# Kernel optimization log

Hardware: AMD Instinct MI355X
Metric: run time of the kernel (lower is better)

Reference implementation:

```python
import jax, jax.numpy as jnp
import numpy as np

N = 50000        # nodes
E = 800000       # edges (before self loops)
F_IN = 78        # num_features_xd
H1 = 10          # heads of gcn1
OUT2 = 128       # output_dim of gcn2
G = 512          # graphs in batch
NEG_SLOPE = 0.2  # PyG GATConv default


def setup_inputs() -> dict:
    key = jax.random.key(0)
    ks = jax.random.split(key, 16)
    def glorot(k, shape, fan_in):
        return jax.random.normal(k, shape, jnp.float32) * (1.0 / np.sqrt(fan_in))
    inp = {}
    inp['x'] = jax.random.normal(ks[0], (N, F_IN), jnp.float32)
    inp['edge_index'] = jax.random.randint(ks[1], (2, E), 0, N, dtype=jnp.int32)
    inp['batch'] = jnp.sort(jax.random.randint(ks[2], (N,), 0, G, dtype=jnp.int32))
    inp['num_graphs'] = G
    # gcn1: GATConv(78 -> 78, heads=10, concat=True)
    inp['W1'] = glorot(ks[3], (F_IN, H1 * F_IN), F_IN)
    inp['a_src1'] = glorot(ks[4], (H1, F_IN), F_IN)
    inp['a_dst1'] = glorot(ks[5], (H1, F_IN), F_IN)
    inp['b1'] = jnp.zeros((H1 * F_IN,), jnp.float32)
    # gcn2: GATConv(780 -> 128, heads=1)
    inp['W2'] = glorot(ks[6], (H1 * F_IN, OUT2), H1 * F_IN)
    inp['a_src2'] = glorot(ks[7], (1, OUT2), OUT2)
    inp['a_dst2'] = glorot(ks[8], (1, OUT2), OUT2)
    inp['b2'] = jnp.zeros((OUT2,), jnp.float32)
    # fc_g1: Linear(128 -> 128)
    inp['fcW'] = glorot(ks[9], (OUT2, OUT2), OUT2)
    inp['fcb'] = jnp.zeros((OUT2,), jnp.float32)
    return inp


def _gat_layer(x, src, dst, W, a_src, a_dst, b, heads, out_dim):
    # x: [N, Fin] -> h: [N, heads, out_dim]
    n = x.shape[0]
    h = (x @ W).reshape(n, heads, out_dim)
    # per-node attention projections: [N, heads]
    alpha_src = jnp.einsum('nhf,hf->nh', h, a_src)
    alpha_dst = jnp.einsum('nhf,hf->nh', h, a_dst)
    # per-edge logits (message from src j to dst i): [Etot, heads]
    e = jax.nn.leaky_relu(alpha_src[src] + alpha_dst[dst], NEG_SLOPE)
    # segment softmax over edges grouped by destination node
    m = jax.ops.segment_max(e, dst, num_segments=n)
    m = jnp.where(jnp.isfinite(m), m, 0.0)
    ex = jnp.exp(e - m[dst])
    denom = jax.ops.segment_sum(ex, dst, num_segments=n)
    alpha = ex / (denom[dst] + 1e-16)
    # weighted message scatter: [N, heads, out_dim]
    out = jax.ops.segment_sum(h[src] * alpha[:, :, None], dst, num_segments=n)
    return out.reshape(n, heads * out_dim) + b


def reference(x, edge_index, batch, num_graphs, W1, a_src1, a_dst1, b1,
              W2, a_src2, a_dst2, b2, fcW, fcb):
    n = x.shape[0]
    # PyG GATConv add_self_loops=True
    loops = jnp.arange(n, dtype=edge_index.dtype)
    src = jnp.concatenate([edge_index[0], loops])
    dst = jnp.concatenate([edge_index[1], loops])
    # eval mode: dropouts are identity
    h = jax.nn.relu(_gat_layer(x, src, dst, W1, a_src1, a_dst1, b1, H1, F_IN))
    h = jax.nn.relu(_gat_layer(h, src, dst, W2, a_src2, a_dst2, b2, 1, OUT2))
    # global max pool over graphs
    pooled = jax.ops.segment_max(h, batch, num_segments=num_graphs)
    pooled = jnp.where(jnp.isfinite(pooled), pooled, 0.0)
    return jax.nn.relu(pooled @ fcW + fcb)
```

## Files before the change

kernel.cpp:

```cpp
#include <hip/hip_runtime.h>
#include <hip/hip_bf16.h>
#include <stdint.h>

typedef unsigned int uint32;
typedef unsigned short u16;
typedef __attribute__((ext_vector_type(8))) short bf16x8;
typedef __attribute__((ext_vector_type(4))) float f32x4;
typedef __attribute__((ext_vector_type(2))) float f32x2;
typedef uint32 u32x4 __attribute__((ext_vector_type(4)));

#define N_NODES 50000
#define NP      50048
#define N_EDGES 800000
#define ETOT    (N_EDGES + N_NODES)
#define F_INN   78
#define H1      10
#define D1      780
#define OUT2    128
#define NGRAPH  512
#define NEG_SLOPE 0.2f
#define PL40    ((size_t)NP * 40)

__device__ __forceinline__ float lrelu(float v) { return v > 0.f ? v : NEG_SLOPE * v; }
__device__ __forceinline__ u16 f2bfbits(float f) {
    return __bfloat16_as_ushort(__float2bfloat16(f));
}
__device__ __forceinline__ uint32 packbf(float lo, float hi) {
    return (uint32)f2bfbits(lo) | ((uint32)f2bfbits(hi) << 16);
}
__device__ __forceinline__ f32x2 bf2(uint32 u) {
    __hip_bfloat162 b = *reinterpret_cast<__hip_bfloat162*>(&u);
    float2 t = __bfloat1622float2(b);
    return (f32x2){t.x, t.y};
}
__device__ __forceinline__ int esrc(const int* ei, int e) { return e < N_EDGES ? ei[e] : e - N_EDGES; }
__device__ __forceinline__ int edst(const int* ei, int e) { return e < N_EDGES ? ei[N_EDGES + e] : e - N_EDGES; }

typedef __attribute__((address_space(1))) const uint32 guint;
typedef __attribute__((address_space(3))) uint32 luint;
__device__ __forceinline__ void cp16(uint32* lds, const uint32* g, int lane) {
    __builtin_amdgcn_global_load_lds((guint*)(g + lane * 4), (luint*)lds, 16, 0, 0);
}

#define NXP (N_NODES * 80)
__global__ __launch_bounds__(256) void prep_kernel(const float* __restrict__ x,
                                                   const float* __restrict__ W1,
                                                   const float* __restrict__ W2,
                                                   u16* __restrict__ xbp,
                                                   u16* __restrict__ w1p,
                                                   u16* __restrict__ w2p) {
    const int total = NXP + 10 * 80 * 80 + 10 * 128 * 80;
    for (int id = blockIdx.x * 256 + threadIdx.x; id < total; id += gridDim.x * 256) {
        if (id < NXP) {
            int n = id / 80, k = id - n * 80;
            xbp[id] = (k < 78) ? f2bfbits(x[n * 78 + k]) : ((k == 78) ? (u16)0x3F80 : (u16)0);
        } else if (id < NXP + 64000) {
            int t = id - NXP;
            int h = t / 6400, r = t - h * 6400;
            int n = r / 80, k = r - n * 80;
            w1p[t] = (n < 78 && k < 78) ? f2bfbits(W1[k * D1 + h * 78 + n]) : (u16)0;
        } else {
            int t = id - NXP - 64000;
            int h = t / 10240, r = t - h * 10240;
            int n = r / 80, k = r - n * 80;
            w2p[t] = (k < 78) ? f2bfbits(W2[(h * 78 + k) * OUT2 + n]) : (u16)0;
        }
    }
}

__global__ __launch_bounds__(256) void prep2_kernel(const float* __restrict__ W1,
                                                    const float* __restrict__ a_src1,
                                                    const float* __restrict__ a_dst1,
                                                    const float* __restrict__ W2,
                                                    const float* __restrict__ a_src2,
                                                    const float* __restrict__ a_dst2,
                                                    u16* __restrict__ VAT,
                                                    float* __restrict__ w2as,
                                                    float* __restrict__ w2ad) {
    int gid = blockIdx.x * 256 + threadIdx.x;
    int gs = gridDim.x * 256;
    for (int idx = gid; idx < 32 * 80; idx += gs) {
        int j = idx / 80, k = idx - j * 80;
        float s = 0.f;
        if (j < 20 && k < 78) {
            int h = (j < 10) ? j : j - 10;
            const float* vec = ((j < 10) ? a_src1 : a_dst1) + h * F_INN;
            const float* wrow = W1 + k * D1 + h * F_INN;
            for (int f = 0; f < F_INN; ++f) s = fmaf(wrow[f], vec[f], s);
            VAT[idx] = f2bfbits(s);
        } else {
            VAT[idx] = 0;
        }
    }
    for (int c = gid; c < D1; c += gs) {
        const float* r0 = W2 + (size_t)c * OUT2;
        float s = 0.f, d = 0.f;
        for (int j = 0; j < OUT2; ++j) {
            s = fmaf(r0[j], a_src2[j], s);
            d = fmaf(r0[j], a_dst2[j], d);
        }
        w2as[c] = s;
        w2ad[c] = d;
    }
}

__global__ __launch_bounds__(256) void alphas1x_kernel(const uint32* __restrict__ xbu,
                                                       const uint32* __restrict__ vatu,
                                                       float* __restrict__ asd1,
                                                       float* __restrict__ asrc) {
    __shared__ uint32 As[5136];
    __shared__ uint32 Bs[1296];
    int tid = threadIdx.x, lane = tid & 63, wv = tid >> 6;
    int row0 = blockIdx.x * 128;
    const uint32* aplane = xbu + (size_t)row0 * 40;

#pragma unroll
    for (int t = 0; t < 5; ++t)
        cp16(As + wv * 1280 + t * 256, aplane + wv * 1280 + t * 256, lane);
    if (wv == 0) {
#pragma unroll
        for (int t = 0; t < 5; ++t)
            cp16(Bs + t * 256, vatu + t * 256, lane);
    }
    __syncthreads();

    int l15 = lane & 15, quad = lane >> 4;
    const u16* Asu = (const u16*)As;
    const u16* Bsu = (const u16*)Bs;
    f32x4 acc[2][2];
#pragma unroll
    for (int mi = 0; mi < 2; ++mi)
#pragma unroll
        for (int nj = 0; nj < 2; ++nj) acc[mi][nj] = (f32x4){0.f, 0.f, 0.f, 0.f};

    int abase[2], bbase[2];
#pragma unroll
    for (int mi = 0; mi < 2; ++mi) abase[mi] = (wv * 32 + mi * 16 + l15) * 80 + quad * 8;
#pragma unroll
    for (int nj = 0; nj < 2; ++nj) bbase[nj] = (nj * 16 + l15) * 80 + quad * 8;

    bf16x8 z8 = {0, 0, 0, 0, 0, 0, 0, 0};
#pragma unroll
    for (int ks = 0; ks < 96; ks += 32) {
        bf16x8 a[2], b[2];
#pragma unroll
        for (int mi = 0; mi < 2; ++mi) {
            a[mi] = *(const bf16x8*)(Asu + abase[mi] + ks);
            if (ks == 64 && quad >= 2) a[mi] = z8;
        }
#pragma unroll
        for (int nj = 0; nj < 2; ++nj) b[nj] = *(const bf16x8*)(Bsu + bbase[nj] + ks);
#pragma unroll
        for (int mi = 0; mi < 2; ++mi)
#pragma unroll
            for (int nj = 0; nj < 2; ++nj)
                acc[mi][nj] = __builtin_amdgcn_mfma_f32_16x16x32_bf16(a[mi], b[nj], acc[mi][nj], 0, 0, 0);
    }

#pragma unroll
    for (int mi = 0; mi < 2; ++mi)
#pragma unroll
        for (int nj = 0; nj < 2; ++nj) {
            int col = nj * 16 + l15;
            if (col < 20) {
#pragma unroll
                for (int reg = 0; reg < 4; ++reg) {
                    int row = row0 + wv * 32 + mi * 16 + quad * 4 + reg;
                    if (row < N_NODES) {
                        asd1[(size_t)row * 20 + col] = acc[mi][nj][reg];
                        if (col < 10) asrc[(size_t)row * 12 + col] = acc[mi][nj][reg];
                    }
                }
            }
        }
}

__global__ void histrank_kernel(const int* __restrict__ ei, int* __restrict__ deg,
                                int* __restrict__ rank) {
    int e = blockIdx.x * 256 + threadIdx.x;
    if (e < ETOT) rank[e] = atomicAdd(&deg[edst(ei, e)], 1);
}

__global__ __launch_bounds__(256) void scan1_kernel(const int* __restrict__ deg,
                                                    int* __restrict__ row_ptr,
                                                    int* __restrict__ bsum) {
    __shared__ int buf[256];
    int tid = threadIdx.x;
    int i = blockIdx.x * 256 + tid;
    int v = (i < N_NODES) ? deg[i] : 0;
    buf[tid] = v;
    __syncthreads();
    for (int off = 1; off < 256; off <<= 1) {
        int t = (tid >= off) ? buf[tid - off] : 0;
        __syncthreads();
        buf[tid] += t;
        __syncthreads();
    }
    if (i < N_NODES) row_ptr[i] = buf[tid] - v;
    if (tid == 255) bsum[blockIdx.x] = buf[255];
}

__global__ __launch_bounds__(256) void scan2_kernel(const int* __restrict__ bsum,
                                                    int* __restrict__ boff) {
    __shared__ int buf[256];
    int tid = threadIdx.x;
    int v = (tid < 196) ? bsum[tid] : 0;
    buf[tid] = v;
    __syncthreads();
    for (int off = 1; off < 256; off <<= 1) {
        int t = (tid >= off) ? buf[tid - off] : 0;
        __syncthreads();
        buf[tid] += t;
        __syncthreads();
    }
    if (tid < 196) boff[tid] = buf[tid] - v;
}

__global__ __launch_bounds__(256) void scan3_kernel(int* __restrict__ row_ptr,
                                                    const int* __restrict__ boff) {
    int i = blockIdx.x * 256 + threadIdx.x;
    if (i < N_NODES) row_ptr[i] = row_ptr[i] + boff[blockIdx.x];
    if (i == 0) row_ptr[N_NODES] = ETOT;
}

__global__ void scatter_kernel(const int* __restrict__ ei, const int* __restrict__ row_ptr,
                               const int* __restrict__ rank, u16* __restrict__ src_arr) {
    int e = blockIdx.x * 256 + threadIdx.x;
    if (e < ETOT) {
        int d = edst(ei, e);
        src_arr[row_ptr[d] + rank[e]] = (u16)esrc(ei, e);
    }
}

__global__ __launch_bounds__(256) void agg1m_kernel(const int* __restrict__ row_ptr,
                                                    const u16* __restrict__ src_arr,
                                                    const float* __restrict__ asrc,
                                                    const float* __restrict__ asd1,
                                                    const uint32* __restrict__ xbu,
                                                    u16* __restrict__ aggb16) {
    __shared__ uint32 S[4][1568];
    int tid = threadIdx.x, lane = tid & 63, wv = tid >> 6;
    int i = blockIdx.x * 4 + wv;
    int rs = row_ptr[i], deg = row_ptr[i + 1] - rs;
    uint32* xt32 = S[wv];
    uint32* wm32 = xt32 + 1280;
    int* sv = (int*)(xt32 + 1536);
    int l15 = lane & 15, quad = lane >> 4;
    int slot = lane & 31, half = lane >> 5;
    u32x4 z4 = {0, 0, 0, 0};
    if (lane < 24) *(u32x4*)(wm32 + 160 + lane * 4) = z4;
    uint32 selv = (l15 & 1) ? 0x07060302u : 0x05040100u;

    float dstv[10];
#pragma unroll
    for (int q = 0; q < 10; ++q) dstv[q] = asd1[(size_t)i * 20 + 10 + q];

    int hp = l15 >> 1;
    int pa1 = (quad * 8 + 4 * hp) & 31;
    int pa2 = (pa1 + 4) & 31;

    f32x4 acc[5];
#pragma unroll
    for (int nt = 0; nt < 5; ++nt) acc[nt] = (f32x4){0.f, 0.f, 0.f, 0.f};

    for (int base = 0; base < deg; base += 32) {
        int cnt = min(deg - base, 32);
        if (lane < cnt) sv[lane] = (int)src_arr[rs + base + lane];
        __builtin_amdgcn_wave_barrier();
        int srow = (slot < cnt) ? sv[slot] : 0;
        const float* arow = asrc + (size_t)srow * 12;
        if (half == 0) {
            float4 a01 = *(const float4*)(arow);
            float2 a2  = *(const float2*)(arow + 4);
            uint32 u0 = 0, u1 = 0, u2 = 0;
            if (slot < cnt) {
                u0 = packbf(__expf(lrelu(a01.x + dstv[0])), __expf(lrelu(a01.y + dstv[1])));
                u1 = packbf(__expf(lrelu(a01.z + dstv[2])), __expf(lrelu(a01.w + dstv[3])));
                u2 = packbf(__expf(lrelu(a2.x + dstv[4])),  __expf(lrelu(a2.y + dstv[5])));
            }
            wm32[0 * 32 + (slot & 31)] = u0;
            wm32[1 * 32 + ((slot + 4) & 31)] = u1;
            wm32[2 * 32 + ((slot + 8) & 31)] = u2;
        } else {
            float2 a3 = *(const float2*)(arow + 6);
            float2 a4 = *(const float2*)(arow + 8);
            uint32 u3 = 0, u4 = 0;
            if (slot < cnt) {
                u3 = packbf(__expf(lrelu(a3.x + dstv[6])), __expf(lrelu(a3.y + dstv[7])));
                u4 = packbf(__expf(lrelu(a4.x + dstv[8])), __expf(lrelu(a4.y + dstv[9])));
            }
            wm32[3 * 32 + ((slot + 12) & 31)] = u3;
            wm32[4 * 32 + ((slot + 16) & 31)] = u4;
        }
#pragma unroll
        for (int t = 0; t < 5; ++t) {
            int c4 = 2 * t + half;
            u32x4 v = z4;
            if (slot < cnt) v = *(const u32x4*)(xbu + (size_t)srow * 40 + c4 * 4);
            uint32* rowp = xt32 + (4 * c4) * 32;
#pragma unroll
            for (int k = 0; k < 4; ++k)
                rowp[k * 32 + ((slot + 16 * c4 + 4 * k) & 31)] = v[k];
        }
        __builtin_amdgcn_wave_barrier();
        int arow2 = hp * 32;
        u32x4 a0 = *(const u32x4*)(wm32 + arow2 + pa1);
        u32x4 a1 = *(const u32x4*)(wm32 + arow2 + pa2);
        u32x4 au = {__builtin_amdgcn_perm(a0[1], a0[0], selv),
                    __builtin_amdgcn_perm(a0[3], a0[2], selv),
                    __builtin_amdgcn_perm(a1[1], a1[0], selv),
                    __builtin_amdgcn_perm(a1[3], a1[2], selv)};
        bf16x8 af = *(bf16x8*)&au;
#pragma unroll
        for (int nt = 0; nt < 5; ++nt) {
            int browb = (nt * 8 + hp) * 32;
            u32x4 b0 = *(const u32x4*)(xt32 + browb + pa1);
            u32x4 b1 = *(const u32x4*)(xt32 + browb + pa2);
            u32x4 bu = {__builtin_amdgcn_perm(b0[1], b0[0], selv),
                        __builtin_amdgcn_perm(b0[3], b0[2], selv),
                        __builtin_amdgcn_perm(b1[1], b1[0], selv),
                        __builtin_amdgcn_perm(b1[3], b1[2], selv)};
            bf16x8 bf = *(bf16x8*)&bu;
            acc[nt] = __builtin_amdgcn_mfma_f32_16x16x32_bf16(af, bf, acc[nt], 0, 0, 0);
        }
        __builtin_amdgcn_wave_barrier();
    }

    float rden[4];
#pragma unroll
    for (int reg = 0; reg < 4; ++reg) {
        float d = __shfl(acc[4][reg], (lane & 48) | 14, 64);
        rden[reg] = __builtin_amdgcn_rcpf(d);
    }
    size_t nb = (size_t)i * 80 + l15;
#pragma unroll
    for (int reg = 0; reg < 4; ++reg) {
        int head = quad * 4 + reg;
        if (head < 10) {
            u16* hpn = aggb16 + (size_t)head * (size_t)PL40 * 2 + nb;
#pragma unroll
            for (int nt = 0; nt < 5; ++nt) {
                float v = acc[nt][reg] * rden[reg];
                u16 b = f2bfbits(v);
                if (nt == 4 && l15 >= 14) b = 0;
                hpn[nt * 16] = b;
            }
        }
    }
}

__global__ __launch_bounds__(256) void gemmf_kernel(const uint32* __restrict__ aggb,
                                                    const uint32* __restrict__ w1p,
                                                    const uint32* __restrict__ w2p,
                                                    const float* __restrict__ b1,
                                                    const float* __restrict__ w2as,
                                                    const float* __restrict__ w2ad,
                                                    u16* __restrict__ h2,
                                                    float* __restrict__ as2,
                                                    float* __restrict__ ad2) {
    __shared__ uint32 As[2576];
    __shared__ uint32 Bs1[3336];
    __shared__ uint32 Bs2[5136];
    __shared__ uint32 C1s[2576];
    int tid = threadIdx.x, lane = tid & 63, wv = tid >> 6;
    int row0 = blockIdx.x * 64;
    int l15 = lane & 15, quad = lane >> 4;
    const u16* Asu = (const u16*)As;
    const u16* B1u = (const u16*)Bs1;
    const u16* B2u = (const u16*)Bs2;
    const u16* C1u = (const u16*)C1s;
    u16* Cw = (u16*)C1s;

    f32x4 acc2[8];
#pragma unroll
    for (int nj = 0; nj < 8; ++nj) acc2[nj] = (f32x4){0.f, 0.f, 0.f, 0.f};
    float s2p[4] = {}, d2p[4] = {};

    int abase = (wv * 16 + l15) * 80 + quad * 8;
    int b1base[5];
#pragma unroll
    for (int nj = 0; nj < 5; ++nj) b1base[nj] = (nj * 16 + l15) * 80 + quad * 8;
    int b2base[8];
#pragma unroll
    for (int nj = 0; nj < 8; ++nj) b2base[nj] = (nj * 16 + l15) * 80 + quad * 8;
    bf16x8 z8 = {0, 0, 0, 0, 0, 0, 0, 0};
    int rl0 = wv * 16 + quad * 4;

    for (int h = 0; h < 10; ++h) {
        const uint32* aplane = aggb + (size_t)h * PL40 + (size_t)row0 * 40;
        const uint32* w1pl = w1p + (size_t)h * 3200;
        const uint32* w2pl = w2p + (size_t)h * 5120;
        for (int t = wv; t < 10; t += 4)
            cp16(As + t * 256, aplane + t * 256, lane);
        int tw0 = wv * 3, tw1 = (wv == 3) ? 13 : wv * 3 + 3;
        for (int t = tw0; t < tw1; ++t)
            cp16(Bs1 + t * 256, w1pl + t * 256, lane);
#pragma unroll
        for (int t = 0; t < 5; ++t)
            cp16(Bs2 + (wv * 5 + t) * 256, w2pl + (wv * 5 + t) * 256, lane);
        __syncthreads();

        f32x4 acc1[5];
#pragma unroll
        for (int nj = 0; nj < 5; ++nj) acc1[nj] = (f32x4){0.f, 0.f, 0.f, 0.f};
#pragma unroll
        for (int ks = 0; ks < 96; ks += 32) {
            bf16x8 a = *(const bf16x8*)(Asu + abase + ks);
            if (ks == 64 && quad >= 2) a = z8;
#pragma unroll
            for (int nj = 0; nj < 5; ++nj) {
                bf16x8 b = *(const bf16x8*)(B1u + b1base[nj] + ks);
                acc1[nj] = __builtin_amdgcn_mfma_f32_16x16x32_bf16(a, b, acc1[nj], 0, 0, 0);
            }
        }
#pragma unroll
        for (int nj = 0; nj < 5; ++nj) {
            int col = nj * 16 + l15;
            if (col < 78) {
                int gc = h * 78 + col;
                float bia = b1[gc], was = w2as[gc], wad = w2ad[gc];
#pragma unroll
                for (int reg = 0; reg < 4; ++reg) {
                    float v = fmaxf(acc1[nj][reg] + bia, 0.f);
                    Cw[(rl0 + reg) * 80 + col] = f2bfbits(v);
                    s2p[reg] = fmaf(v, was, s2p[reg]);
                    d2p[reg] = fmaf(v, wad, d2p[reg]);
                }
            } else {
#pragma unroll
                for (int reg = 0; reg < 4; ++reg) Cw[(rl0 + reg) * 80 + col] = 0;
            }
        }
        __builtin_amdgcn_wave_barrier();
#pragma unroll
        for (int ks = 0; ks < 96; ks += 32) {
            bf16x8 a = *(const bf16x8*)(C1u + abase + ks);
            if (ks == 64 && quad >= 2) a = z8;
#pragma unroll
            for (int nj = 0; nj < 8; ++nj) {
                bf16x8 b = *(const bf16x8*)(B2u + b2base[nj] + ks);
                acc2[nj] = __builtin_amdgcn_mfma_f32_16x16x32_bf16(a, b, acc2[nj], 0, 0, 0);
            }
        }
        __syncthreads();
    }

#pragma unroll
    for (int nj = 0; nj < 8; ++nj) {
        int col = nj * 16 + l15;
#pragma unroll
        for (int reg = 0; reg < 4; ++reg) {
            int r = row0 + rl0 + reg;
            if (r < N_NODES) h2[(size_t)r * OUT2 + col] = f2bfbits(acc2[nj][reg]);
        }
    }
#pragma unroll
    for (int off = 1; off < 16; off <<= 1)
#pragma unroll
        for (int reg = 0; reg < 4; ++reg) {
            s2p[reg] += __shfl_xor(s2p[reg], off, 64);
            d2p[reg] += __shfl_xor(d2p[reg], off, 64);
        }
    if (l15 == 0) {
#pragma unroll
        for (int reg = 0; reg < 4; ++reg) {
            int r = row0 + rl0 + reg;
            if (r < N_NODES) {
                as2[r] = s2p[reg];
                ad2[r] = d2p[reg];
            }
        }
    }
}

__global__ __launch_bounds__(256) void agg2_kernel(const int* __restrict__ row_ptr,
                                                   const u16* __restrict__ src_arr,
                                                   const float* __restrict__ as2,
                                                   const float* __restrict__ ad2,
                                                   const uint32* __restrict__ h2u,
                                                   const float* __restrict__ b2,
                                                   const int* __restrict__ batch,
                                                   float* __restrict__ pooled) {
    __shared__ float w_sh[4][64];
    __shared__ int src_sh[4][64];
    __shared__ float red[4][128];
    __shared__ int gsh[4];
    int tid = threadIdx.x, lane = tid & 63, wv = tid >> 6;
    int i = blockIdx.x * 4 + wv;
    int rs = row_ptr[i], deg = row_ptr[i + 1] - rs;
    float ad2i = ad2[i];

    f32x2 acc = {0.f, 0.f};
    float den = 0.f;
    if (deg <= 64) {
        if (lane < deg) {
            int s = (int)src_arr[rs + lane];
            float w = __expf(lrelu(as2[s] + ad2i));
            den = w;
            w_sh[wv][lane] = w;
            src_sh[wv][lane] = s;
        }
        __builtin_amdgcn_wave_barrier();
#pragma unroll
        for (int off = 1; off < 64; off <<= 1) den += __shfl_xor(den, off, 64);
        float rden = __builtin_amdgcn_rcpf(den);
        int cnt = deg, eix = 0;
        for (; eix + 7 < cnt; eix += 8) {
            int ss[8];
            float ww[8];
            uint32 uu[8];
#pragma unroll
            for (int q = 0; q < 8; ++q) {
                ss[q] = src_sh[wv][eix + q];
                ww[q] = w_sh[wv][eix + q];
            }
#pragma unroll
            for (int q = 0; q < 8; ++q) uu[q] = h2u[(size_t)ss[q] * 64 + lane];
#pragma unroll
            for (int q = 0; q < 8; ++q) acc = ww[q] * bf2(uu[q]) + acc;
        }
        for (; eix < cnt; ++eix) {
            int s0 = src_sh[wv][eix];
            float w0 = w_sh[wv][eix];
            uint32 u0 = h2u[(size_t)s0 * 64 + lane];
            acc = w0 * bf2(u0) + acc;
        }
        acc *= rden;
    } else {
        for (int eix = lane; eix < deg; eix += 64)
            den += __expf(lrelu(as2[(int)src_arr[rs + eix]] + ad2i));
#pragma unroll
        for (int off = 1; off < 64; off <<= 1) den += __shfl_xor(den, off, 64);
        float rden = __builtin_amdgcn_rcpf(den);
        for (int base = 0; base < deg; base += 64) {
            int cnt = min(deg - base, 64);
            if (lane < cnt) {
                int s = (int)src_arr[rs + base + lane];
                w_sh[wv][lane] = __expf(lrelu(as2[s] + ad2i));
                src_sh[wv][lane] = s;
            }
            __builtin_amdgcn_wave_barrier();
            int eix = 0;
            for (; eix + 7 < cnt; eix += 8) {
                int ss[8];
                float ww[8];
                uint32 uu[8];
#pragma unroll
                for (int q = 0; q < 8; ++q) {
                    ss[q] = src_sh[wv][eix + q];
                    ww[q] = w_sh[wv][eix + q];
                }
#pragma unroll
                for (int q = 0; q < 8; ++q) uu[q] = h2u[(size_t)ss[q] * 64 + lane];
#pragma unroll
                for (int q = 0; q < 8; ++q) acc = ww[q] * bf2(uu[q]) + acc;
            }
            for (; eix < cnt; ++eix) {
                int s0 = src_sh[wv][eix];
                float w0 = w_sh[wv][eix];
                uint32 u0 = h2u[(size_t)s0 * 64 + lane];
                acc = w0 * bf2(u0) + acc;
            }
            __builtin_amdgcn_wave_barrier();
        }
        acc *= rden;
    }
    float2 bv = ((const float2*)b2)[lane];
    float v0 = fmaxf(acc.x + bv.x, 0.f);
    float v1 = fmaxf(acc.y + bv.y, 0.f);
    int g = batch[i];
    red[wv][2 * lane] = v0;
    red[wv][2 * lane + 1] = v1;
    if (lane == 0) gsh[wv] = g;
    __syncthreads();
    bool leader = true;
#pragma unroll
    for (int w2i = 0; w2i < 3; ++w2i)
        if (w2i < wv && gsh[w2i] == g) leader = false;
    if (leader) {
        float m0 = v0, m1 = v1;
#pragma unroll
        for (int w2i = 1; w2i < 4; ++w2i) {
            if (w2i > wv && gsh[w2i] == g) {
                m0 = fmaxf(m0, red[w2i][2 * lane]);
                m1 = fmaxf(m1, red[w2i][2 * lane + 1]);
            }
        }
        atomicMax((int*)&pooled[g * OUT2 + 2 * lane], __float_as_int(m0));
        atomicMax((int*)&pooled[g * OUT2 + 2 * lane + 1], __float_as_int(m1));
    }
}

__global__ __launch_bounds__(128) void fc_kernel(const float* __restrict__ pooled,
                                                 const float* __restrict__ fcW,
                                                 const float* __restrict__ fcb,
                                                 float* __restrict__ out) {
    int g = blockIdx.x, tid = threadIdx.x;
    __shared__ float p[128];
    p[tid] = pooled[g * OUT2 + tid];
    __syncthreads();
    float acc = fcb[tid];
    for (int k = 0; k < 128; ++k) acc = fmaf(p[k], fcW[k * OUT2 + tid], acc);
    out[g * OUT2 + tid] = fmaxf(acc, 0.f);
}

extern "C" void kernel_launch(void* const* d_in, const int* in_sizes, int n_in,
                              void* d_out, int out_size, void* d_ws, size_t ws_size,
                              hipStream_t stream) {
    const float* x      = (const float*)d_in[0];
    const int*   ei     = (const int*)d_in[1];
    const int*   batch  = (const int*)d_in[2];
    const float* W1     = (const float*)d_in[4];
    const float* a_src1 = (const float*)d_in[5];
    const float* a_dst1 = (const float*)d_in[6];
    const float* b1     = (const float*)d_in[7];
    const float* W2     = (const float*)d_in[8];
    const float* a_src2 = (const float*)d_in[9];
    const float* a_dst2 = (const float*)d_in[10];
    const float* b2     = (const float*)d_in[11];
    const float* fcW    = (const float*)d_in[12];
    const float* fcb    = (const float*)d_in[13];
    float* out = (float*)d_out;

    size_t off = 0;
    char* base = (char*)d_ws;
    auto alloc = [&](size_t bytes) -> void* {
        void* p = base + off;
        off += (bytes + 255) & ~(size_t)255;
        return p;
    };
    uint32* aggb  = (uint32*)alloc(PL40 * 10 * 4);
    u16* h2arena  = (u16*)alloc((size_t)N_NODES * OUT2 * 2);
    u16* h2   = h2arena;
    u16* xbp  = h2arena;
    float* asd1 = (float*)alloc((size_t)N_NODES * 20 * 4);
    float* asrc = (float*)alloc((size_t)N_NODES * 12 * 4);
    float* as2  = (float*)alloc((size_t)N_NODES * 4);
    float* ad2  = (float*)alloc((size_t)N_NODES * 4);
    u16* w1p    = (u16*)alloc((size_t)(10 * 80 * 80) * 2 + 1024);
    u16* w2p    = (u16*)alloc((size_t)(10 * 128 * 80) * 2);
    u16* VAT    = (u16*)alloc((size_t)32 * 80 * 2);
    float* w2as = (float*)alloc((size_t)D1 * 4);
    float* w2ad = (float*)alloc((size_t)D1 * 4);
    float* pooled = (float*)alloc((size_t)NGRAPH * OUT2 * 4);
    int* deg     = (int*)alloc((size_t)N_NODES * 4);
    int* row_ptr = (int*)alloc((size_t)(N_NODES + 1) * 4);
    int* rank    = (int*)alloc((size_t)ETOT * 4);
    u16* src_arr = (u16*)alloc((size_t)ETOT * 2);
    int* bsum    = (int*)alloc(196 * 4);
    int* boff    = (int*)alloc(196 * 4);

    hipMemsetAsync(deg, 0, (size_t)N_NODES * 4, stream);
    hipMemsetAsync(pooled, 0, (size_t)NGRAPH * OUT2 * 4, stream);

    prep_kernel<<<2048, 256, 0, stream>>>(x, W1, W2, xbp, w1p, w2p);
    prep2_kernel<<<8, 256, 0, stream>>>(W1, a_src1, a_dst1, W2, a_src2, a_dst2,
                                        VAT, w2as, w2ad);
    alphas1x_kernel<<<391, 256, 0, stream>>>((const uint32*)xbp, (const uint32*)VAT,
                                             asd1, asrc);
    histrank_kernel<<<(ETOT + 255) / 256, 256, 0, stream>>>(ei, deg, rank);
    scan1_kernel<<<196, 256, 0, stream>>>(deg, row_ptr, bsum);
    scan2_kernel<<<1, 256, 0, stream>>>(bsum, boff);
    scan3_kernel<<<196, 256, 0, stream>>>(row_ptr, boff);
    scatter_kernel<<<(ETOT + 255) / 256, 256, 0, stream>>>(ei, row_ptr, rank, src_arr);
    agg1m_kernel<<<N_NODES / 4, 256, 0, stream>>>(row_ptr, src_arr, asrc, asd1,
                                                  (const uint32*)xbp, (u16*)aggb);
    gemmf_kernel<<<NP / 64, 256, 0, stream>>>(aggb, (const uint32*)w1p, (const uint32*)w2p,
                                              b1, w2as, w2ad, h2, as2, ad2);
    agg2_kernel<<<N_NODES / 4, 256, 0, stream>>>(row_ptr, src_arr, as2, ad2,
                                                 (const uint32*)h2, b2, batch, pooled);
    fc_kernel<<<NGRAPH, 128, 0, stream>>>(pooled, fcW, fcb, out);
}
```

Measured before the change: 316.5 us.

## Process two destination nodes per wave in GAT layer-1 aggregation with prefetched gathers

Each wave now aggregates two destination nodes instead of one, halving the grid. When both nodes have degree at most 32, the source-row gathers for the second node are issued before the MFMA and write-out of the first, overlapping gather latency with compute. Source indices are read directly into registers instead of through a shared-memory staging array. This raises register pressure and halves the number of waves, and src_arr is read unconditionally past the row end for inactive lanes.

```diff
diff --git a/kernel.cpp b/kernel.cpp
--- a/kernel.cpp
+++ b/kernel.cpp
@@ -232,62 +232,75 @@
     }
 }
 
+struct G1 {
+    float4 a01; float2 a2;
+    float2 a3, a4;
+    u32x4 xv[5];
+    int valid;
+};
+
 __global__ __launch_bounds__(256) void agg1m_kernel(const int* __restrict__ row_ptr,
                                                     const u16* __restrict__ src_arr,
                                                     const float* __restrict__ asrc,
                                                     const float* __restrict__ asd1,
                                                     const uint32* __restrict__ xbu,
                                                     u16* __restrict__ aggb16) {
-    __shared__ uint32 S[4][1568];
+    __shared__ uint32 S[4][1536];
     int tid = threadIdx.x, lane = tid & 63, wv = tid >> 6;
-    int i = blockIdx.x * 4 + wv;
-    int rs = row_ptr[i], deg = row_ptr[i + 1] - rs;
+    int ip = blockIdx.x * 4 + wv;
+    int i0 = ip * 2, i1 = i0 + 1;
+    int rs0 = row_ptr[i0], d0 = row_ptr[i0 + 1] - rs0;
+    int rs1 = row_ptr[i1], d1 = row_ptr[i1 + 1] - rs1;
     uint32* xt32 = S[wv];
     uint32* wm32 = xt32 + 1280;
-    int* sv = (int*)(xt32 + 1536);
     int l15 = lane & 15, quad = lane >> 4;
     int slot = lane & 31, half = lane >> 5;
     u32x4 z4 = {0, 0, 0, 0};
     if (lane < 24) *(u32x4*)(wm32 + 160 + lane * 4) = z4;
     uint32 selv = (l15 & 1) ? 0x07060302u : 0x05040100u;
-
-    float dstv[10];
-#pragma unroll
-    for (int q = 0; q < 10; ++q) dstv[q] = asd1[(size_t)i * 20 + 10 + q];
-
     int hp = l15 >> 1;
     int pa1 = (quad * 8 + 4 * hp) & 31;
     int pa2 = (pa1 + 4) & 31;
 
-    f32x4 acc[5];
-#pragma unroll
-    for (int nt = 0; nt < 5; ++nt) acc[nt] = (f32x4){0.f, 0.f, 0.f, 0.f};
-
-    for (int base = 0; base < deg; base += 32) {
-        int cnt = min(deg - base, 32);
-        if (lane < cnt) sv[lane] = (int)src_arr[rs + base + lane];
-        __builtin_amdgcn_wave_barrier();
-        int srow = (slot < cnt) ? sv[slot] : 0;
+    float dstv0[10], dstv1[10];
+#pragma unroll
+    for (int q = 0; q < 10; ++q) dstv0[q] = asd1[(size_t)i0 * 20 + 10 + q];
+#pragma unroll
+    for (int q = 0; q < 10; ++q) dstv1[q] = asd1[(size_t)i1 * 20 + 10 + q];
+
+    auto gatherrows = [&](int s, int cnt, G1& g) {
+        g.valid = slot < cnt;
+        int srow = g.valid ? s : 0;
         const float* arow = asrc + (size_t)srow * 12;
         if (half == 0) {
-            float4 a01 = *(const float4*)(arow);
-            float2 a2  = *(const float2*)(arow + 4);
+            if (g.valid) { g.a01 = *(const float4*)(arow); g.a2 = *(const float2*)(arow + 4); }
+        } else {
+            if (g.valid) { g.a3 = *(const float2*)(arow + 6); g.a4 = *(const float2*)(arow + 8); }
+        }
+#pragma unroll
+        for (int t = 0; t < 5; ++t) {
+            int c4 = 2 * t + half;
+            g.xv[t] = z4;
+            if (g.valid) g.xv[t] = *(const u32x4*)(xbu + (size_t)srow * 40 + c4 * 4);
+        }
+    };
+
+    auto stage = [&](const G1& g, const float* dstv) {
+        if (half == 0) {
             uint32 u0 = 0, u1 = 0, u2 = 0;
-            if (slot < cnt) {
-                u0 = packbf(__expf(lrelu(a01.x + dstv[0])), __expf(lrelu(a01.y + dstv[1])));
-                u1 = packbf(__expf(lrelu(a01.z + dstv[2])), __expf(lrelu(a01.w + dstv[3])));
-                u2 = packbf(__expf(lrelu(a2.x + dstv[4])),  __expf(lrelu(a2.y + dstv[5])));
+            if (g.valid) {
+                u0 = packbf(__expf(lrelu(g.a01.x + dstv[0])), __expf(lrelu(g.a01.y + dstv[1])));
+                u1 = packbf(__expf(lrelu(g.a01.z + dstv[2])), __expf(lrelu(g.a01.w + dstv[3])));
+                u2 = packbf(__expf(lrelu(g.a2.x + dstv[4])),  __expf(lrelu(g.a2.y + dstv[5])));
             }
             wm32[0 * 32 + (slot & 31)] = u0;
             wm32[1 * 32 + ((slot + 4) & 31)] = u1;
             wm32[2 * 32 + ((slot + 8) & 31)] = u2;
         } else {
-            float2 a3 = *(const float2*)(arow + 6);
-            float2 a4 = *(const float2*)(arow + 8);
             uint32 u3 = 0, u4 = 0;
-            if (slot < cnt) {
-                u3 = packbf(__expf(lrelu(a3.x + dstv[6])), __expf(lrelu(a3.y + dstv[7])));
-                u4 = packbf(__expf(lrelu(a4.x + dstv[8])), __expf(lrelu(a4.y + dstv[9])));
+            if (g.valid) {
+                u3 = packbf(__expf(lrelu(g.a3.x + dstv[6])), __expf(lrelu(g.a3.y + dstv[7])));
+                u4 = packbf(__expf(lrelu(g.a4.x + dstv[8])), __expf(lrelu(g.a4.y + dstv[9])));
             }
             wm32[3 * 32 + ((slot + 12) & 31)] = u3;
             wm32[4 * 32 + ((slot + 16) & 31)] = u4;
@@ -295,14 +308,14 @@
 #pragma unroll
         for (int t = 0; t < 5; ++t) {
             int c4 = 2 * t + half;
-            u32x4 v = z4;
-            if (slot < cnt) v = *(const u32x4*)(xbu + (size_t)srow * 40 + c4 * 4);
             uint32* rowp = xt32 + (4 * c4) * 32;
 #pragma unroll
             for (int k = 0; k < 4; ++k)
-                rowp[k * 32 + ((slot + 16 * c4 + 4 * k) & 31)] = v[k];
-        }
-        __builtin_amdgcn_wave_barrier();
+                rowp[k * 32 + ((slot + 16 * c4 + 4 * k) & 31)] = g.xv[t][k];
+        }
+    };
+
+    auto domfma = [&](f32x4* acc) {
         int arow2 = hp * 32;
         u32x4 a0 = *(const u32x4*)(wm32 + arow2 + pa1);
         u32x4 a1 = *(const u32x4*)(wm32 + arow2 + pa2);
@@ -323,28 +336,68 @@
             bf16x8 bf = *(bf16x8*)&bu;
             acc[nt] = __builtin_amdgcn_mfma_f32_16x16x32_bf16(af, bf, acc[nt], 0, 0, 0);
         }
+    };
+
+    auto writeout = [&](int i, f32x4* acc) {
+        float rden[4];
+#pragma unroll
+        for (int reg = 0; reg < 4; ++reg) {
+            float d = __shfl(acc[4][reg], (lane & 48) | 14, 64);
+            rden[reg] = __builtin_amdgcn_rcpf(d);
+        }
+        size_t nb = (size_t)i * 80 + l15;
+#pragma unroll
+        for (int reg = 0; reg < 4; ++reg) {
+            int head = quad * 4 + reg;
+            if (head < 10) {
+                u16* hpn = aggb16 + (size_t)head * (size_t)PL40 * 2 + nb;
+#pragma unroll
+                for (int nt = 0; nt < 5; ++nt) {
+                    float v = acc[nt][reg] * rden[reg];
+                    u16 b = f2bfbits(v);
+                    if (nt == 4 && l15 >= 14) b = 0;
+                    hpn[nt * 16] = b;
+                }
+            }
+        }
+    };
+
+    f32x4 acc0[5], acc1[5];
+#pragma unroll
+    for (int nt = 0; nt < 5; ++nt) { acc0[nt] = (f32x4){0.f,0.f,0.f,0.f}; acc1[nt] = (f32x4){0.f,0.f,0.f,0.f}; }
+
+    if (d0 <= 32 && d1 <= 32) {
+        int s0 = (int)src_arr[rs0 + slot];
+        int s1 = (int)src_arr[rs1 + slot];
+        G1 g0, g1;
+        gatherrows(s0, d0, g0);
+        stage(g0, dstv0);
+        gatherrows(s1, d1, g1);
         __builtin_amdgcn_wave_barrier();
-    }
-
-    float rden[4];
-#pragma unroll
-    for (int reg = 0; reg < 4; ++reg) {
-        float d = __shfl(acc[4][reg], (lane & 48) | 14, 64);
-        rden[reg] = __builtin_amdgcn_rcpf(d);
-    }
-    size_t nb = (size_t)i * 80 + l15;
-#pragma unroll
-    for (int reg = 0; reg < 4; ++reg) {
-        int head = quad * 4 + reg;
-        if (head < 10) {
-            u16* hpn = aggb16 + (size_t)head * (size_t)PL40 * 2 + nb;
-#pragma unroll
-            for (int nt = 0; nt < 5; ++nt) {
-                float v = acc[nt][reg] * rden[reg];
-                u16 b = f2bfbits(v);
-                if (nt == 4 && l15 >= 14) b = 0;
-                hpn[nt * 16] = b;
-            }
+        domfma(acc0);
+        writeout(i0, acc0);
+        __builtin_amdgcn_wave_barrier();
+        stage(g1, dstv1);
+        __builtin_amdgcn_wave_barrier();
+        domfma(acc1);
+        writeout(i1, acc1);
+    } else {
+        int rss[2] = {rs0, rs1}, dd[2] = {d0, d1}, ii[2] = {i0, i1};
+#pragma unroll
+        for (int n = 0; n < 2; ++n) {
+            f32x4* acc = (n == 0) ? acc0 : acc1;
+            const float* dv = (n == 0) ? dstv0 : dstv1;
+            for (int base = 0; base < dd[n]; base += 32) {
+                int cnt = min(dd[n] - base, 32);
+                int s = (int)src_arr[rss[n] + base + slot];
+                G1 g;
+                gatherrows(s, cnt, g);
+                stage(g, dv);
+                __builtin_amdgcn_wave_barrier();
+                domfma(acc);
+                __builtin_amdgcn_wave_barrier();
+            }
+            writeout(ii[n], acc);
         }
     }
 }
@@ -663,7 +716,7 @@
     scan2_kernel<<<1, 256, 0, stream>>>(bsum, boff);
     scan3_kernel<<<196, 256, 0, stream>>>(row_ptr, boff);
     scatter_kernel<<<(ETOT + 255) / 256, 256, 0, stream>>>(ei, row_ptr, rank, src_arr);
-    agg1m_kernel<<<N_NODES / 4, 256, 0, stream>>>(row_ptr, src_arr, asrc, asd1,
+    agg1m_kernel<<<N_NODES / 8, 256, 0, stream>>>(row_ptr, src_arr, asrc, asd1,
                                                   (const uint32*)xbp, (u16*)aggb);
     gemmf_kernel<<<NP / 64, 256, 0, stream>>>(aggb, (const uint32*)w1p, (const uint32*)w2p,
                                               b1, w2as, w2ad, h2, as2, ad2);
```

Measured after the change: 317.3 us. Within noise of the previous version (+0.3%).
